# Kernel optimization log

Hardware: AMD Instinct MI355X
Metric: run time of the kernel (lower is better)

The kernel has to match this reference:

```python
import jax, jax.numpy as jnp
import numpy as np

B, T, F_IN, H, NCLS = 4096, 48, 225, 128, 100


def _lstm_scan(xg, whh):
    """xg: [T, B, 4H] precomputed input-gate contributions (incl. biases).
    whh: [4H, H]. Returns hidden states [T, B, H]. PyTorch gate order i,f,g,o."""
    h_dim = whh.shape[1]
    b = xg.shape[1]

    def step(carry, g_x):
        h, c = carry
        gates = g_x + h @ whh.T  # [B, 4H]
        i, f, g, o = jnp.split(gates, 4, axis=-1)
        i = jax.nn.sigmoid(i)
        f = jax.nn.sigmoid(f)
        g = jnp.tanh(g)
        o = jax.nn.sigmoid(o)
        c = f * c + i * g
        h = o * jnp.tanh(c)
        return (h, c), h

    init = (jnp.zeros((b, h_dim), xg.dtype), jnp.zeros((b, h_dim), xg.dtype))
    _, hs = jax.lax.scan(step, init, xg)
    return hs  # [T, B, H]


def setup_inputs() -> dict:
    key = jax.random.key(0)
    ks = jax.random.split(key, 14)
    s = 1.0 / np.sqrt(H)  # PyTorch LSTM init scale
    rnd = lambda k, shape, sc: (jax.random.uniform(k, shape, jnp.float32) * 2 - 1) * sc
    return {
        "x": jax.random.normal(ks[0], (B, T, F_IN), jnp.float32),
        "w_ih_fwd": rnd(ks[1], (4 * H, F_IN), s),
        "w_hh_fwd": rnd(ks[2], (4 * H, H), s),
        "b_ih_fwd": rnd(ks[3], (4 * H,), s),
        "b_hh_fwd": rnd(ks[4], (4 * H,), s),
        "w_ih_bwd": rnd(ks[5], (4 * H, F_IN), s),
        "w_hh_bwd": rnd(ks[6], (4 * H, H), s),
        "b_ih_bwd": rnd(ks[7], (4 * H,), s),
        "b_hh_bwd": rnd(ks[8], (4 * H,), s),
        "fc1_w": rnd(ks[9], (128, 2 * H), 1.0 / np.sqrt(2 * H)),
        "fc1_b": rnd(ks[10], (128,), 1.0 / np.sqrt(2 * H)),
        "fc2_w": rnd(ks[11], (NCLS, 128), 1.0 / np.sqrt(128)),
        "fc2_b": rnd(ks[12], (NCLS,), 1.0 / np.sqrt(128)),
    }


def reference(x, w_ih_fwd, w_hh_fwd, b_ih_fwd, b_hh_fwd,
              w_ih_bwd, w_hh_bwd, b_ih_bwd, b_hh_bwd,
              fc1_w, fc1_b, fc2_w, fc2_b):
    # Precompute input projections for all timesteps: [B,T,4H] -> [T,B,4H]
    xg_f = (jnp.einsum('btf,gf->btg', x, w_ih_fwd) + b_ih_fwd + b_hh_fwd).transpose(1, 0, 2)
    hs_f = _lstm_scan(xg_f, w_hh_fwd)  # [T,B,H]

    x_rev = x[:, ::-1, :]
    xg_b = (jnp.einsum('btf,gf->btg', x_rev, w_ih_bwd) + b_ih_bwd + b_hh_bwd).transpose(1, 0, 2)
    hs_b = _lstm_scan(xg_b, w_hh_bwd)[::-1]  # reverse back to forward time order

    lstm_out = jnp.concatenate([hs_f, hs_b], axis=-1)  # [T,B,2H]
    pooled = jnp.mean(lstm_out, axis=0)  # [B,2H] (temporal mean)
    # Dropout is identity in eval mode.
    h1 = jax.nn.relu(pooled @ fc1_w.T + fc1_b)
    logits = h1 @ fc2_w.T + fc2_b  # [B, NCLS]
    return logits
```

## Files before the change

### kernel.cpp

```cpp
#include <hip/hip_runtime.h>
#include <stdint.h>

#define NB 4096
#define NT 48
#define NF 225
#define NH 128
#define NG 512
#define NK 256
#define NCLS 100

typedef __attribute__((ext_vector_type(8))) _Float16 v8h;
typedef __attribute__((ext_vector_type(4))) _Float16 v4h;
typedef __attribute__((ext_vector_type(4))) float v4f;

__device__ __forceinline__ float fsig(float x) {
    return __builtin_amdgcn_rcpf(1.f + __expf(-x));
}
__device__ __forceinline__ float ftanh(float x) {
    return 2.f * __builtin_amdgcn_rcpf(1.f + __expf(-2.f * x)) - 1.f;
}
__device__ __forceinline__ int opq(int x) { asm volatile("" : "+v"(x)); return x; }

__device__ __forceinline__ void mfma_ba(v4f& c, v8h a, v8h b) {
    asm volatile("v_mfma_f32_16x16x32_f16 %0, %1, %2, %0"
                 : "+v"(c) : "v"(a), "a"(b));
}
__device__ __forceinline__ void mfma_bv(v4f& c, v8h a, v8h b) {
    asm volatile("v_mfma_f32_16x16x32_f16 %0, %1, %2, %0"
                 : "+v"(c) : "v"(a), "v"(b));
}

__device__ __forceinline__ void gld16(const void* g, void* l) {
    __builtin_amdgcn_global_load_lds(
        (const __attribute__((address_space(1))) void*)g,
        (__attribute__((address_space(3))) void*)l, 16, 0, 0);
}

__global__ __launch_bounds__(256) void k_prep(
    const float* __restrict__ x,
    const float* __restrict__ wihf, const float* __restrict__ wihb,
    const float* __restrict__ whhf, const float* __restrict__ whhb,
    const float* __restrict__ bihf, const float* __restrict__ bhhf,
    const float* __restrict__ bihb, const float* __restrict__ bhhb,
    _Float16* __restrict__ xh, _Float16* __restrict__ wt,
    _Float16* __restrict__ wht, _Float16* __restrict__ wh3,
    _Float16* __restrict__ whh3, float* __restrict__ bsum)
{
    __shared__ __attribute__((aligned(16))) _Float16 ls[NT * NF + 16];
    const int bid = blockIdx.x;
    const int tid = threadIdx.x;

    if (bid < NB) {
        const float* src = x + (size_t)bid * (NT * NF);
        for (int i = tid; i < (NT * NF) / 4; i += 256) {
            const float4 v = ((const float4*)src)[i];
            v4h hv; hv[0] = (_Float16)v.x; hv[1] = (_Float16)v.y;
            hv[2] = (_Float16)v.z; hv[3] = (_Float16)v.w;
            *(v4h*)(ls + i * 4) = hv;
        }
        __syncthreads();
        const int key = bid & 7;
        for (int task = tid; task < NT * 32; task += 256) {
            const int t = task >> 5, c = task & 31;
            v8h hv;
#pragma unroll
            for (int e = 0; e < 8; ++e) {
                const int k = c * 8 + e;
                hv[e] = (k < NF) ? ls[t * NF + k] : (_Float16)0.f;
            }
            *(v8h*)(xh + ((size_t)t * NB + bid) * NK + ((c ^ key) << 3)) = hv;
        }
    } else if (bid < NB + 96) {
        const int task = (bid - NB) * 256 + tid;
        const int n = task % 384;
        const int r2 = task / 384;
        const int grp = r2 & 3, ks = (r2 >> 2) & 7, dir = r2 >> 5;
        const float* src = (dir ? wihb : wihf) + (size_t)n * NF;
        v8h hv;
#pragma unroll
        for (int e = 0; e < 8; ++e) {
            const int k = ks * 32 + grp * 8 + e;
            hv[e] = (k < NF) ? (_Float16)src[k] : (_Float16)0.f;
        }
        *(v8h*)(wt + (size_t)task * 8) = hv;
    } else if (bid < NB + 144) {
        const int task = (bid - NB - 96) * 256 + tid;
        const int n = task % 384;
        const int r2 = task / 384;
        const int grp = r2 & 3, ks = (r2 >> 2) & 3, dir = r2 >> 4;
        const float* src = (dir ? whhb : whhf) + (size_t)n * NH + ks * 32 + grp * 8;
        v8h hv;
#pragma unroll
        for (int e = 0; e < 8; ++e) hv[e] = (_Float16)src[e];
        *(v8h*)(wht + (size_t)task * 8) = hv;
    } else if (bid < NB + 148) {
        for (int s = 0; s < 8; ++s) {
            const int task = (bid - NB - 144) * 2048 + s * 256 + tid;
            const int dir = task >> 12;
            const int rem = task & 4095;
            const int col = rem >> 5, c = rem & 31;
            const float* src = (dir ? wihb : wihf) + (size_t)(384 + col) * NF + c * 8;
            v8h hv;
#pragma unroll
            for (int e = 0; e < 8; ++e) {
                const int k = c * 8 + e;
                hv[e] = (k < NF) ? (_Float16)src[e] : (_Float16)0.f;
            }
            *(v8h*)(wh3 + ((size_t)dir * 128 + col) * NK + ((c ^ (col & 7)) << 3)) = hv;
        }
    } else if (bid < NB + 150) {
        for (int s = 0; s < 8; ++s) {
            const int task = (bid - NB - 148) * 2048 + s * 256 + tid;
            const int dir = task >> 11;
            const int rem = task & 2047;
            const int col = rem >> 4, c = rem & 15;
            const float* src = (dir ? whhb : whhf) + (size_t)(384 + col) * NH + c * 8;
            v8h hv;
#pragma unroll
            for (int e = 0; e < 8; ++e) hv[e] = (_Float16)src[e];
            *(v8h*)(whh3 + ((size_t)dir * 128 + col) * NH + ((c ^ (col & 7)) << 3)) = hv;
        }
    } else {
        for (int i = tid; i < 1024; i += 256) {
            const int dir = i >> 9, n = i & 511;
            bsum[i] = dir ? (bihb[n] + bhhb[n]) : (bihf[n] + bhhf[n]);
        }
    }
}

__global__ void __launch_bounds__(512, 2) k_fused(
    const _Float16* __restrict__ xh,
    const _Float16* __restrict__ wt,
    const _Float16* __restrict__ wht,
    const _Float16* __restrict__ wh3,
    const _Float16* __restrict__ whh3,
    const float* __restrict__ bsum,
    float* __restrict__ hsum)
{
    __shared__ __attribute__((aligned(16))) _Float16 xb[2][32 * 256];
    __shared__ __attribute__((aligned(16))) _Float16 hb[2][32 * 128];
    __shared__ __attribute__((aligned(16))) _Float16 bxo[128 * 256];
    __shared__ __attribute__((aligned(16))) _Float16 bho[128 * 128];

    const int tid   = threadIdx.x;
    const int btile = blockIdx.x;
    const int dir   = blockIdx.y;
    const int rb    = btile * 32;
    const int lane  = tid & 63;
    const int w     = tid >> 6;
    const int l15   = lane & 15;
    const int grp   = lane >> 4;
    const int hcol  = w * 16 + l15;
    const int swz   = hcol & 7;

#pragma unroll
    for (int j = 0; j < 12; ++j) {
        const int seg = w + j * 8;
        if (seg < 64)
            gld16((const char*)wh3 + (size_t)dir * 65536 + (seg << 10) + lane * 16,
                  (char*)bxo + (seg << 10));
        else
            gld16((const char*)whh3 + (size_t)dir * 32768 + ((seg - 64) << 10) + lane * 16,
                  (char*)bho + ((seg - 64) << 10));
    }

    v8h bx[3][8], bh[3][4];
#pragma unroll
    for (int g = 0; g < 3; ++g) {
#pragma unroll
        for (int ks = 0; ks < 8; ++ks) {
            bx[g][ks] = *(const v8h*)(wt +
                ((((size_t)dir * 8 + ks) * 4 + grp) * 384 + g * 128 + hcol) * 8);
            asm volatile("" : "+a"(bx[g][ks]));
        }
#pragma unroll
        for (int ks = 0; ks < 4; ++ks) {
            bh[g][ks] = *(const v8h*)(wht +
                ((((size_t)dir * 4 + ks) * 4 + grp) * 384 + g * 128 + hcol) * 8);
            asm volatile("" : "+a"(bh[g][ks]));
        }
    }
    float bias[4];
#pragma unroll
    for (int g = 0; g < 4; ++g)
        bias[g] = bsum[dir * NG + g * NH + hcol];

    float c0[2][4], hs0[2][4];
#pragma unroll
    for (int m = 0; m < 2; ++m)
#pragma unroll
        for (int r = 0; r < 4; ++r) { c0[m][r] = 0.f; hs0[m][r] = 0.f; }

    auto stage = [&](int tx, int buf) {
        const char* src = (const char*)(xh + ((size_t)tx * NB + rb) * NK);
#pragma unroll
        for (int c = 0; c < 2; ++c) {
            const int seg = w * 2 + c;
            gld16(src + (seg << 10) + lane * 16, (char*)xb[buf] + (seg << 10));
        }
    };

    stage(dir ? (NT - 1) : 0, 0);
    __syncthreads();

    int cur = 0, hc = 0;
#pragma unroll 1
    for (int t = 0; t < NT; ++t) {
        if (t + 1 < NT)
            stage(dir ? (NT - 2 - t) : (t + 1), cur ^ 1);

        v4f acc[2][4];
#pragma unroll
        for (int m = 0; m < 2; ++m)
#pragma unroll
            for (int g = 0; g < 4; ++g)
                acc[m][g] = (v4f){bias[g], bias[g], bias[g], bias[g]};

        asm volatile("s_nop 2"
            : "+v"(acc[0][0]), "+v"(acc[0][1]), "+v"(acc[0][2]), "+v"(acc[0][3]),
              "+v"(acc[1][0]), "+v"(acc[1][1]), "+v"(acc[1][2]), "+v"(acc[1][3]));

#pragma unroll
        for (int ks = 0; ks < 8; ++ks) {
            const int ch = ((ks * 4 + grp) ^ swz) << 4;
            v8h af0 = *(const v8h*)((const char*)xb[cur] + (l15 << 9)
                        + ((((ks * 4 + grp) ^ (l15 & 7))) << 4));
            v8h af1 = *(const v8h*)((const char*)xb[cur] + ((16 + l15) << 9)
                        + ((((ks * 4 + grp) ^ (l15 & 7))) << 4));
            v8h bo = *(const v8h*)((const char*)bxo + opq((hcol << 9) + ch));
            mfma_ba(acc[0][0], af0, bx[0][ks]);
            mfma_ba(acc[1][0], af1, bx[0][ks]);
            mfma_ba(acc[0][1], af0, bx[1][ks]);
            mfma_ba(acc[1][1], af1, bx[1][ks]);
            mfma_ba(acc[0][2], af0, bx[2][ks]);
            mfma_ba(acc[1][2], af1, bx[2][ks]);
            mfma_bv(acc[0][3], af0, bo);
            mfma_bv(acc[1][3], af1, bo);
        }

        if (t > 0) {
#pragma unroll
            for (int ks = 0; ks < 4; ++ks) {
                const int ch = ((ks * 4 + grp) ^ swz) << 4;
                v8h ah0 = *(const v8h*)((const char*)hb[hc] + (l15 << 8)
                            + ((((ks * 4 + grp) ^ (l15 & 7))) << 4));
                v8h ah1 = *(const v8h*)((const char*)hb[hc] + ((16 + l15) << 8)
                            + ((((ks * 4 + grp) ^ (l15 & 7))) << 4));
                v8h bo2 = *(const v8h*)((const char*)bho + opq((hcol << 8) + ch));
                mfma_ba(acc[0][0], ah0, bh[0][ks]);
                mfma_ba(acc[1][0], ah1, bh[0][ks]);
                mfma_ba(acc[0][1], ah0, bh[1][ks]);
                mfma_ba(acc[1][1], ah1, bh[1][ks]);
                mfma_ba(acc[0][2], ah0, bh[2][ks]);
                mfma_ba(acc[1][2], ah1, bh[2][ks]);
                mfma_bv(acc[0][3], ah0, bo2);
                mfma_bv(acc[1][3], ah1, bo2);
            }
        }

        asm volatile("s_nop 7\n\ts_nop 7"
            : "+v"(acc[0][0]), "+v"(acc[0][1]), "+v"(acc[0][2]), "+v"(acc[0][3]),
              "+v"(acc[1][0]), "+v"(acc[1][1]), "+v"(acc[1][2]), "+v"(acc[1][3]));

#pragma unroll
        for (int m = 0; m < 2; ++m)
#pragma unroll
            for (int r = 0; r < 4; ++r) {
                const float iv = fsig(acc[m][0][r]);
                const float fv = fsig(acc[m][1][r]);
                const float gv = ftanh(acc[m][2][r]);
                const float ov = fsig(acc[m][3][r]);
                const float c = fv * c0[m][r] + iv * gv;
                c0[m][r] = c;
                const float h = ov * ftanh(c);
                hs0[m][r] += h;
                const int b = m * 16 + grp * 4 + r;
                const int byo = (b << 8) + ((hcol << 1) ^ ((b & 7) << 4));
                *(_Float16*)((char*)hb[hc ^ 1] + byo) = (_Float16)h;
            }
        __syncthreads();
        cur ^= 1; hc ^= 1;
    }

#pragma unroll
    for (int m = 0; m < 2; ++m)
#pragma unroll
        for (int r = 0; r < 4; ++r)
            hsum[((size_t)dir * NB + rb + m * 16 + grp * 4 + r) * NH + hcol] =
                hs0[m][r];
}

__global__ __launch_bounds__(128) void k_head(
    const float* __restrict__ hsum,
    const float* __restrict__ fc1w, const float* __restrict__ fc1b,
    const float* __restrict__ fc2w, const float* __restrict__ fc2b,
    float* __restrict__ out)
{
    __shared__ __attribute__((aligned(16))) float pooled[16][256];
    __shared__ __attribute__((aligned(16))) float h1s[16][128];
    __shared__ __attribute__((aligned(16))) char wbuf[65536];

    const int tid = threadIdx.x;
    const int rb  = blockIdx.x * 16;

    for (int i = tid; i < 16 * 256; i += 128) {
        const int r = i >> 8, c = i & 255;
        const float v = (c < 128)
            ? hsum[(size_t)(rb + r) * NH + c]
            : hsum[((size_t)NB + rb + r) * NH + (c - 128)];
        pooled[r][c] = v * (1.f / (float)NT);
    }
    for (int i = tid; i < 128 * 64; i += 128) {
        const int j = i >> 6, kq = i & 63;
        const float4 v = *(const float4*)(fc1w + (size_t)j * 256 + (kq << 2));
        v4h pv; pv[0] = (_Float16)v.x; pv[1] = (_Float16)v.y;
        pv[2] = (_Float16)v.z; pv[3] = (_Float16)v.w;
        const int byo = (j << 9) + ((kq << 3) ^ (((j >> 3) & 7) << 4));
        *(v4h*)(wbuf + byo) = pv;
    }
    __syncthreads();

    const int rgrp = tid >> 4;
    const int joct = tid & 15;
    const int r0 = rgrp * 2;
    const int j0 = joct * 8;

    float a1[2][8];
#pragma unroll
    for (int rr = 0; rr < 2; ++rr)
#pragma unroll
        for (int jo = 0; jo < 8; ++jo) a1[rr][jo] = 0.f;

    for (int kc = 0; kc < 32; ++kc) {
        const int k = kc << 3;
        float pv[2][8];
#pragma unroll
        for (int rr = 0; rr < 2; ++rr) {
            const float4 pa = *(const float4*)&pooled[r0 + rr][k];
            const float4 pb = *(const float4*)&pooled[r0 + rr][k + 4];
            pv[rr][0] = pa.x; pv[rr][1] = pa.y; pv[rr][2] = pa.z; pv[rr][3] = pa.w;
            pv[rr][4] = pb.x; pv[rr][5] = pb.y; pv[rr][6] = pb.z; pv[rr][7] = pb.w;
        }
#pragma unroll
        for (int jo = 0; jo < 8; ++jo) {
            const int j = j0 + jo;
            const int byo = (j << 9) + ((k << 1) ^ (((j >> 3) & 7) << 4));
            const v8h wv = *(const v8h*)(wbuf + byo);
#pragma unroll
            for (int i = 0; i < 8; ++i) {
                const float wf = (float)wv[i];
#pragma unroll
                for (int rr = 0; rr < 2; ++rr)
                    a1[rr][jo] += pv[rr][i] * wf;
            }
        }
    }
#pragma unroll
    for (int rr = 0; rr < 2; ++rr)
#pragma unroll
        for (int jo = 0; jo < 8; ++jo) {
            const int j = j0 + jo;
            const float v = a1[rr][jo] + fc1b[j];
            h1s[r0 + rr][j] = v > 0.f ? v : 0.f;
        }
    __syncthreads();

    for (int i = tid; i < 100 * 32; i += 128) {
        const int j = i >> 5, kq = i & 31;
        const float4 v = *(const float4*)(fc2w + (size_t)j * 128 + (kq << 2));
        const int byo = (j << 9) + ((kq << 4) ^ (((j >> 3) & 7) << 4));
        *(float4*)(wbuf + byo) = v;
    }
    __syncthreads();

    if (j0 < 100) {
        float a2[2][8];
#pragma unroll
        for (int rr = 0; rr < 2; ++rr)
#pragma unroll
            for (int jo = 0; jo < 8; ++jo) a2[rr][jo] = 0.f;

        for (int kc = 0; kc < 16; ++kc) {
            const int k = kc << 3;
            float hv[2][8];
#pragma unroll
            for (int rr = 0; rr < 2; ++rr) {
                const float4 ha = *(const float4*)&h1s[r0 + rr][k];
                const float4 hbv = *(const float4*)&h1s[r0 + rr][k + 4];
                hv[rr][0] = ha.x; hv[rr][1] = ha.y; hv[rr][2] = ha.z; hv[rr][3] = ha.w;
                hv[rr][4] = hbv.x; hv[rr][5] = hbv.y; hv[rr][6] = hbv.z; hv[rr][7] = hbv.w;
            }
#pragma unroll
            for (int jo = 0; jo < 8; ++jo) {
                const int j = j0 + jo;
                if (j < 100) {
                    const int sw = ((j >> 3) & 7) << 4;
                    const float4 wa = *(const float4*)(wbuf + (j << 9) + ((k << 2) ^ sw));
                    const float4 wb = *(const float4*)(wbuf + (j << 9) + (((k + 4) << 2) ^ sw));
#pragma unroll
                    for (int rr = 0; rr < 2; ++rr) {
                        a2[rr][jo] += hv[rr][0] * wa.x + hv[rr][1] * wa.y
                                    + hv[rr][2] * wa.z + hv[rr][3] * wa.w
                                    + hv[rr][4] * wb.x + hv[rr][5] * wb.y
                                    + hv[rr][6] * wb.z + hv[rr][7] * wb.w;
                    }
                }
            }
        }
#pragma unroll
        for (int rr = 0; rr < 2; ++rr)
#pragma unroll
            for (int jo = 0; jo < 8; ++jo) {
                const int j = j0 + jo;
                if (j < 100)
                    out[(size_t)(rb + r0 + rr) * NCLS + j] = a2[rr][jo] + fc2b[j];
            }
    }
}

extern "C" void kernel_launch(void* const* d_in, const int* in_sizes, int n_in,
                              void* d_out, int out_size, void* d_ws, size_t ws_size,
                              hipStream_t stream)
{
    (void)in_sizes; (void)n_in; (void)out_size; (void)ws_size;
    const float* x    = (const float*)d_in[0];
    const float* wihf = (const float*)d_in[1];
    const float* whhf = (const float*)d_in[2];
    const float* bihf = (const float*)d_in[3];
    const float* bhhf = (const float*)d_in[4];
    const float* wihb = (const float*)d_in[5];
    const float* whhb = (const float*)d_in[6];
    const float* bihb = (const float*)d_in[7];
    const float* bhhb = (const float*)d_in[8];
    const float* fc1w = (const float*)d_in[9];
    const float* fc1b = (const float*)d_in[10];
    const float* fc2w = (const float*)d_in[11];
    const float* fc2b = (const float*)d_in[12];
    float* out = (float*)d_out;

    char* ws = (char*)d_ws;
    float*     hs    = (float*)ws;
    size_t off = (size_t)4 * 1024 * 1024;
    _Float16*  xh    = (_Float16*)(ws + off); off += (size_t)NB * NT * NK * 2;
    _Float16*  wt    = (_Float16*)(ws + off); off += (size_t)2 * 8 * 4 * 384 * 8 * 2;
    _Float16*  wht   = (_Float16*)(ws + off); off += (size_t)2 * 4 * 4 * 384 * 8 * 2;
    _Float16*  wh3   = (_Float16*)(ws + off); off += (size_t)2 * 128 * NK * 2;
    _Float16*  whh3  = (_Float16*)(ws + off); off += (size_t)2 * 128 * NH * 2;
    float*     bsum  = (float*)(ws + off);    off += 1024 * 4;

    k_prep<<<dim3(NB + 151), dim3(256), 0, stream>>>(
        x, wihf, wihb, whhf, whhb, bihf, bhhf, bihb, bhhb,
        xh, wt, wht, wh3, whh3, bsum);
    k_fused<<<dim3(128, 2), dim3(512), 0, stream>>>(
        xh, wt, wht, wh3, whh3, bsum, hs);
    k_head<<<dim3(256), dim3(128), 0, stream>>>(hs, fc1w, fc1b, fc2w, fc2b, out);
}
```

Measured before the change: 267.1 us.

## Fuse fp32 input conversion into LSTM kernel and drop the fp16 staging pass

Removes the per-batch conversion of x to a padded, transposed fp16 buffer from the prep kernel. The recurrent kernel now streams fp32 x straight into LDS with 4-byte global_load_lds, using a swizzled layout, and packs it to fp16 in registers before the MFMAs. It also reorders each step: the recurrent h·Whh MFMAs for step t+1 run right after the barrier while that step's x load is in flight, which lets the kernel use single LDS buffers. The intent is to avoid writing and re-reading a large intermediate tensor. In exchange there are narrower global loads, extra convert instructions and an extra barrier per step, and the padded K columns now read neighbouring data that is masked only by zero weights.

```diff
diff --git a/kernel.cpp b/kernel.cpp
--- a/kernel.cpp
+++ b/kernel.cpp
@@ -6,11 +6,11 @@
 #define NF 225
 #define NH 128
 #define NG 512
-#define NK 256
 #define NCLS 100
 
 typedef __attribute__((ext_vector_type(8))) _Float16 v8h;
 typedef __attribute__((ext_vector_type(4))) _Float16 v4h;
+typedef __attribute__((ext_vector_type(2))) __fp16 v2hf;
 typedef __attribute__((ext_vector_type(4))) float v4f;
 
 __device__ __forceinline__ float fsig(float x) {
@@ -35,43 +35,35 @@
         (const __attribute__((address_space(1))) void*)g,
         (__attribute__((address_space(3))) void*)l, 16, 0, 0);
 }
+__device__ __forceinline__ void gld4(const void* g, void* l) {
+    __builtin_amdgcn_global_load_lds(
+        (const __attribute__((address_space(1))) void*)g,
+        (__attribute__((address_space(3))) void*)l, 4, 0, 0);
+}
+
+__device__ __forceinline__ v8h pack8(v4f a, v4f b) {
+    union { v2hf h2[4]; v8h h8; } u;
+    u.h2[0] = __builtin_amdgcn_cvt_pkrtz(a[0], a[1]);
+    u.h2[1] = __builtin_amdgcn_cvt_pkrtz(a[2], a[3]);
+    u.h2[2] = __builtin_amdgcn_cvt_pkrtz(b[0], b[1]);
+    u.h2[3] = __builtin_amdgcn_cvt_pkrtz(b[2], b[3]);
+    return u.h8;
+}
 
 __global__ __launch_bounds__(256) void k_prep(
-    const float* __restrict__ x,
     const float* __restrict__ wihf, const float* __restrict__ wihb,
     const float* __restrict__ whhf, const float* __restrict__ whhb,
     const float* __restrict__ bihf, const float* __restrict__ bhhf,
     const float* __restrict__ bihb, const float* __restrict__ bhhb,
-    _Float16* __restrict__ xh, _Float16* __restrict__ wt,
-    _Float16* __restrict__ wht, _Float16* __restrict__ wh3,
-    _Float16* __restrict__ whh3, float* __restrict__ bsum)
+    _Float16* __restrict__ wt, _Float16* __restrict__ wht,
+    _Float16* __restrict__ wh3, _Float16* __restrict__ whh3,
+    float* __restrict__ bsum)
 {
-    __shared__ __attribute__((aligned(16))) _Float16 ls[NT * NF + 16];
     const int bid = blockIdx.x;
     const int tid = threadIdx.x;
 
-    if (bid < NB) {
-        const float* src = x + (size_t)bid * (NT * NF);
-        for (int i = tid; i < (NT * NF) / 4; i += 256) {
-            const float4 v = ((const float4*)src)[i];
-            v4h hv; hv[0] = (_Float16)v.x; hv[1] = (_Float16)v.y;
-            hv[2] = (_Float16)v.z; hv[3] = (_Float16)v.w;
-            *(v4h*)(ls + i * 4) = hv;
-        }
-        __syncthreads();
-        const int key = bid & 7;
-        for (int task = tid; task < NT * 32; task += 256) {
-            const int t = task >> 5, c = task & 31;
-            v8h hv;
-#pragma unroll
-            for (int e = 0; e < 8; ++e) {
-                const int k = c * 8 + e;
-                hv[e] = (k < NF) ? ls[t * NF + k] : (_Float16)0.f;
-            }
-            *(v8h*)(xh + ((size_t)t * NB + bid) * NK + ((c ^ key) << 3)) = hv;
-        }
-    } else if (bid < NB + 96) {
-        const int task = (bid - NB) * 256 + tid;
+    if (bid < 96) {
+        const int task = bid * 256 + tid;
         const int n = task % 384;
         const int r2 = task / 384;
         const int grp = r2 & 3, ks = (r2 >> 2) & 7, dir = r2 >> 5;
@@ -83,8 +75,8 @@
             hv[e] = (k < NF) ? (_Float16)src[k] : (_Float16)0.f;
         }
         *(v8h*)(wt + (size_t)task * 8) = hv;
-    } else if (bid < NB + 144) {
-        const int task = (bid - NB - 96) * 256 + tid;
+    } else if (bid < 144) {
+        const int task = (bid - 96) * 256 + tid;
         const int n = task % 384;
         const int r2 = task / 384;
         const int grp = r2 & 3, ks = (r2 >> 2) & 3, dir = r2 >> 4;
@@ -93,9 +85,9 @@
 #pragma unroll
         for (int e = 0; e < 8; ++e) hv[e] = (_Float16)src[e];
         *(v8h*)(wht + (size_t)task * 8) = hv;
-    } else if (bid < NB + 148) {
+    } else if (bid < 148) {
         for (int s = 0; s < 8; ++s) {
-            const int task = (bid - NB - 144) * 2048 + s * 256 + tid;
+            const int task = (bid - 144) * 2048 + s * 256 + tid;
             const int dir = task >> 12;
             const int rem = task & 4095;
             const int col = rem >> 5, c = rem & 31;
@@ -106,11 +98,11 @@
                 const int k = c * 8 + e;
                 hv[e] = (k < NF) ? (_Float16)src[e] : (_Float16)0.f;
             }
-            *(v8h*)(wh3 + ((size_t)dir * 128 + col) * NK + ((c ^ (col & 7)) << 3)) = hv;
-        }
-    } else if (bid < NB + 150) {
+            *(v8h*)(wh3 + ((size_t)dir * 128 + col) * 256 + ((c ^ (col & 7)) << 3)) = hv;
+        }
+    } else if (bid < 150) {
         for (int s = 0; s < 8; ++s) {
-            const int task = (bid - NB - 148) * 2048 + s * 256 + tid;
+            const int task = (bid - 148) * 2048 + s * 256 + tid;
             const int dir = task >> 11;
             const int rem = task & 2047;
             const int col = rem >> 4, c = rem & 15;
@@ -129,7 +121,7 @@
 }
 
 __global__ void __launch_bounds__(512, 2) k_fused(
-    const _Float16* __restrict__ xh,
+    const float* __restrict__ xg,
     const _Float16* __restrict__ wt,
     const _Float16* __restrict__ wht,
     const _Float16* __restrict__ wh3,
@@ -137,8 +129,8 @@
     const float* __restrict__ bsum,
     float* __restrict__ hsum)
 {
-    __shared__ __attribute__((aligned(16))) _Float16 xb[2][32 * 256];
-    __shared__ __attribute__((aligned(16))) _Float16 hb[2][32 * 128];
+    __shared__ __attribute__((aligned(16))) float    xbf[32 * 256];
+    __shared__ __attribute__((aligned(16))) _Float16 hb[32 * 128];
     __shared__ __attribute__((aligned(16))) _Float16 bxo[128 * 256];
     __shared__ __attribute__((aligned(16))) _Float16 bho[128 * 128];
 
@@ -152,6 +144,8 @@
     const int grp   = lane >> 4;
     const int hcol  = w * 16 + l15;
     const int swz   = hcol & 7;
+    const int P0    = ((lane >> 2) << 4) | ((lane & 3) << 2);
+    const int xlim  = NB * NT * NF * 4 - 4;
 
 #pragma unroll
     for (int j = 0; j < 12; ++j) {
@@ -191,42 +185,52 @@
 #pragma unroll
         for (int r = 0; r < 4; ++r) { c0[m][r] = 0.f; hs0[m][r] = 0.f; }
 
-    auto stage = [&](int tx, int buf) {
-        const char* src = (const char*)(xh + ((size_t)tx * NB + rb) * NK);
-#pragma unroll
-        for (int c = 0; c < 2; ++c) {
-            const int seg = w * 2 + c;
-            gld16(src + (seg << 10) + lane * 16, (char*)xb[buf] + (seg << 10));
+    auto stagex = [&](int tt) {
+        const int tx = dir ? (NT - 1 - tt) : tt;
+#pragma unroll
+        for (int rr = 0; rr < 4; ++rr) {
+            const int row = w * 4 + rr;
+            const int keysh = (row & 7) << 4;
+            const int gb = (rb + row) * 43200 + tx * 900;
+#pragma unroll
+            for (int win = 0; win < 4; ++win) {
+                int voff = gb + (win << 8) + (P0 ^ keysh);
+                voff = voff < xlim ? voff : xlim;
+                gld4((const char*)xg + voff,
+                     (char*)xbf + (row << 10) + (win << 8));
+            }
         }
     };
 
-    stage(dir ? (NT - 1) : 0, 0);
+    v4f acc[2][4];
+#pragma unroll
+    for (int m = 0; m < 2; ++m)
+#pragma unroll
+        for (int g = 0; g < 4; ++g)
+            acc[m][g] = (v4f){bias[g], bias[g], bias[g], bias[g]};
+
+    stagex(0);
     __syncthreads();
 
-    int cur = 0, hc = 0;
+    const int key = l15 & 7;
+
 #pragma unroll 1
     for (int t = 0; t < NT; ++t) {
-        if (t + 1 < NT)
-            stage(dir ? (NT - 2 - t) : (t + 1), cur ^ 1);
-
-        v4f acc[2][4];
-#pragma unroll
-        for (int m = 0; m < 2; ++m)
-#pragma unroll
-            for (int g = 0; g < 4; ++g)
-                acc[m][g] = (v4f){bias[g], bias[g], bias[g], bias[g]};
-
         asm volatile("s_nop 2"
             : "+v"(acc[0][0]), "+v"(acc[0][1]), "+v"(acc[0][2]), "+v"(acc[0][3]),
               "+v"(acc[1][0]), "+v"(acc[1][1]), "+v"(acc[1][2]), "+v"(acc[1][3]));
 
 #pragma unroll
         for (int ks = 0; ks < 8; ++ks) {
+            const int G0 = ks * 8 + grp * 2;
+            const v4f fa0 = *(const v4f*)(xbf + (l15 << 8) + ((G0 ^ key) << 2));
+            const v4f fb0 = *(const v4f*)(xbf + (l15 << 8) + (((G0 + 1) ^ key) << 2));
+            const v4f fa1 = *(const v4f*)(xbf + ((16 + l15) << 8) + ((G0 ^ key) << 2));
+            const v4f fb1 = *(const v4f*)(xbf + ((16 + l15) << 8) + (((G0 + 1) ^ key) << 2));
+            v8h af0 = pack8(fa0, fb0);
+            v8h af1 = pack8(fa1, fb1);
+            asm volatile("s_nop 1" : "+v"(af0), "+v"(af1));
             const int ch = ((ks * 4 + grp) ^ swz) << 4;
-            v8h af0 = *(const v8h*)((const char*)xb[cur] + (l15 << 9)
-                        + ((((ks * 4 + grp) ^ (l15 & 7))) << 4));
-            v8h af1 = *(const v8h*)((const char*)xb[cur] + ((16 + l15) << 9)
-                        + ((((ks * 4 + grp) ^ (l15 & 7))) << 4));
             v8h bo = *(const v8h*)((const char*)bxo + opq((hcol << 9) + ch));
             mfma_ba(acc[0][0], af0, bx[0][ks]);
             mfma_ba(acc[1][0], af1, bx[0][ks]);
@@ -236,26 +240,6 @@
             mfma_ba(acc[1][2], af1, bx[2][ks]);
             mfma_bv(acc[0][3], af0, bo);
             mfma_bv(acc[1][3], af1, bo);
-        }
-
-        if (t > 0) {
-#pragma unroll
-            for (int ks = 0; ks < 4; ++ks) {
-                const int ch = ((ks * 4 + grp) ^ swz) << 4;
-                v8h ah0 = *(const v8h*)((const char*)hb[hc] + (l15 << 8)
-                            + ((((ks * 4 + grp) ^ (l15 & 7))) << 4));
-                v8h ah1 = *(const v8h*)((const char*)hb[hc] + ((16 + l15) << 8)
-                            + ((((ks * 4 + grp) ^ (l15 & 7))) << 4));
-                v8h bo2 = *(const v8h*)((const char*)bho + opq((hcol << 8) + ch));
-                mfma_ba(acc[0][0], ah0, bh[0][ks]);
-                mfma_ba(acc[1][0], ah1, bh[0][ks]);
-                mfma_ba(acc[0][1], ah0, bh[1][ks]);
-                mfma_ba(acc[1][1], ah1, bh[1][ks]);
-                mfma_ba(acc[0][2], ah0, bh[2][ks]);
-                mfma_ba(acc[1][2], ah1, bh[2][ks]);
-                mfma_bv(acc[0][3], ah0, bo2);
-                mfma_bv(acc[1][3], ah1, bo2);
-            }
         }
 
         asm volatile("s_nop 7\n\ts_nop 7"
@@ -276,10 +260,40 @@
                 hs0[m][r] += h;
                 const int b = m * 16 + grp * 4 + r;
                 const int byo = (b << 8) + ((hcol << 1) ^ ((b & 7) << 4));
-                *(_Float16*)((char*)hb[hc ^ 1] + byo) = (_Float16)h;
+                *(_Float16*)((char*)hb + byo) = (_Float16)h;
             }
         __syncthreads();
-        cur ^= 1; hc ^= 1;
+
+        if (t + 1 < NT) {
+            stagex(t + 1);
+
+#pragma unroll
+            for (int m = 0; m < 2; ++m)
+#pragma unroll
+                for (int g = 0; g < 4; ++g)
+                    acc[m][g] = (v4f){bias[g], bias[g], bias[g], bias[g]};
+            asm volatile("s_nop 2"
+                : "+v"(acc[0][0]), "+v"(acc[0][1]), "+v"(acc[0][2]), "+v"(acc[0][3]),
+                  "+v"(acc[1][0]), "+v"(acc[1][1]), "+v"(acc[1][2]), "+v"(acc[1][3]));
+#pragma unroll
+            for (int ks = 0; ks < 4; ++ks) {
+                const int ch = ((ks * 4 + grp) ^ swz) << 4;
+                v8h ah0 = *(const v8h*)((const char*)hb + (l15 << 8)
+                            + ((((ks * 4 + grp) ^ key)) << 4));
+                v8h ah1 = *(const v8h*)((const char*)hb + ((16 + l15) << 8)
+                            + ((((ks * 4 + grp) ^ key)) << 4));
+                v8h bo2 = *(const v8h*)((const char*)bho + opq((hcol << 8) + ch));
+                mfma_ba(acc[0][0], ah0, bh[0][ks]);
+                mfma_ba(acc[1][0], ah1, bh[0][ks]);
+                mfma_ba(acc[0][1], ah0, bh[1][ks]);
+                mfma_ba(acc[1][1], ah1, bh[1][ks]);
+                mfma_ba(acc[0][2], ah0, bh[2][ks]);
+                mfma_ba(acc[1][2], ah1, bh[2][ks]);
+                mfma_bv(acc[0][3], ah0, bo2);
+                mfma_bv(acc[1][3], ah1, bo2);
+            }
+            __syncthreads();
+        }
     }
 
 #pragma unroll
@@ -441,17 +455,16 @@
     char* ws = (char*)d_ws;
     float*     hs    = (float*)ws;
     size_t off = (size_t)4 * 1024 * 1024;
-    _Float16*  xh    = (_Float16*)(ws + off); off += (size_t)NB * NT * NK * 2;
     _Float16*  wt    = (_Float16*)(ws + off); off += (size_t)2 * 8 * 4 * 384 * 8 * 2;
     _Float16*  wht   = (_Float16*)(ws + off); off += (size_t)2 * 4 * 4 * 384 * 8 * 2;
-    _Float16*  wh3   = (_Float16*)(ws + off); off += (size_t)2 * 128 * NK * 2;
+    _Float16*  wh3   = (_Float16*)(ws + off); off += (size_t)2 * 128 * 256 * 2;
     _Float16*  whh3  = (_Float16*)(ws + off); off += (size_t)2 * 128 * NH * 2;
     float*     bsum  = (float*)(ws + off);    off += 1024 * 4;
 
-    k_prep<<<dim3(NB + 151), dim3(256), 0, stream>>>(
-        x, wihf, wihb, whhf, whhb, bihf, bhhf, bihb, bhhb,
-        xh, wt, wht, wh3, whh3, bsum);
+    k_prep<<<dim3(151), dim3(256), 0, stream>>>(
+        wihf, wihb, whhf, whhb, bihf, bhhf, bihb, bhhb,
+        wt, wht, wh3, whh3, bsum);
     k_fused<<<dim3(128, 2), dim3(512), 0, stream>>>(
-        xh, wt, wht, wh3, whh3, bsum, hs);
+        x, wt, wht, wh3, whh3, bsum, hs);
     k_head<<<dim3(256), dim3(128), 0, stream>>>(hs, fc1w, fc1b, fc2w, fc2b, out);
 }
```

After: 425.5 us. +59.3%, slower.
